# Kernel optimization log

Measured on AMD Instinct MI355X. Metric: run time of the kernel, lower is better.

## Reference

```python
import jax, jax.numpy as jnp
import numpy as np

B, N, DIM, H, D, S = 4, 16384, 256, 8, 64, 64
INNER = H * D


def setup_inputs() -> dict:
    key = jax.random.key(0)
    ks = jax.random.split(key, 10)
    f = lambda k, shp, s: jax.random.normal(k, shp, jnp.float32) * s
    return {
        "x": jax.random.normal(ks[0], (B, N, DIM), jnp.float32),
        "Wx": f(ks[1], (INNER, DIM), 0.02), "bx": jnp.zeros((INNER,), jnp.float32),
        "Wfx": f(ks[2], (INNER, DIM), 0.02), "bfx": jnp.zeros((INNER,), jnp.float32),
        "Wslice": f(ks[3], (S, D), 0.125), "bslice": jnp.zeros((S,), jnp.float32),
        "temperature": jnp.full((1, H, 1, 1), 0.5, jnp.float32),
        "Wq": f(ks[4], (D, D), 0.125),
        "Wk": f(ks[5], (D, D), 0.125),
        "Wv": f(ks[6], (D, D), 0.125),
        "attn_scale": jnp.full((1, H, 1, 1), 10.0, jnp.float32),
        "slice_res_scale": jnp.full((1,), 0.1, jnp.float32),
        "Wout": f(ks[7], (DIM, INNER), 0.02), "bout": jnp.zeros((DIM,), jnp.float32),
    }


def reference(x, Wx, bx, Wfx, bfx, Wslice, bslice, temperature,
              Wq, Wk, Wv, attn_scale, slice_res_scale, Wout, bout):
    b, n, _ = x.shape
    # project and split heads -> [b, h, n, d]
    fx = (x @ Wfx.T + bfx).reshape(b, n, H, D).transpose(0, 2, 1, 3)
    xm = (x @ Wx.T + bx).reshape(b, n, H, D).transpose(0, 2, 1, 3)
    temp = jnp.clip(temperature, 1e-4)
    slice_logits = (xm @ Wslice.T + bslice) / temp              # [b,h,n,S]
    w = jax.nn.softmax(slice_logits, axis=-1)                   # slice weights
    slice_norm = w.sum(axis=2)                                  # [b,h,S]
    tok = jnp.einsum('bhnc,bhng->bhgc', fx, w)                  # [b,h,S,d]
    tok = tok / (slice_norm + 1e-5)[:, :, :, None]
    # small cross-slice attention (cosine, shared kv across heads)
    q = tok @ Wq.T                                              # [b,h,S,d]
    kv = tok.mean(axis=1, keepdims=True)                        # [b,1,S,d]
    k = kv @ Wk.T
    v = kv @ Wv.T
    qn = q / jnp.maximum(jnp.linalg.norm(q, axis=-1, keepdims=True), 1e-12)
    kn = k / jnp.maximum(jnp.linalg.norm(k, axis=-1, keepdims=True), 1e-12)
    logits = jnp.einsum('bhgd,bzsd->bhgs', qn, kn) * attn_scale  # z==1 broadcast
    attn = jax.nn.softmax(logits, axis=-1)
    out_tok = jnp.einsum('bhgs,bzsd->bhgd', attn, v)
    out_tok = out_tok + slice_res_scale * tok
    # broadcast slice tokens back to points
    out_x = jnp.einsum('bhgc,bhng->bhnc', out_tok, w)           # [b,h,n,d]
    out_x = out_x.transpose(0, 2, 1, 3).reshape(b, n, H * D)
    return out_x @ Wout.T + bout
```

## Files before the change

kernel.cpp:

```cpp
#include <hip/hip_runtime.h>
#include <math.h>

#define BQ   4
#define NTOK 16384
#define DIMM 256
#define HH   8
#define DDIM 64
#define SSL  64
#define INNERD 512
#define BN_TOK (BQ*NTOK)

typedef __attribute__((ext_vector_type(8))) short short8;
typedef __attribute__((ext_vector_type(4))) float f32x4;

__device__ inline float bf2f(unsigned short u) {
    union { float f; unsigned int i; } v; v.i = ((unsigned int)u) << 16; return v.f;
}
__device__ inline unsigned short f2bf(float f) {
    union { float f; unsigned int i; } v; v.f = f;
    unsigned int r = v.i + 0x7FFFu + ((v.i >> 16) & 1u);
    return (unsigned short)(r >> 16);
}

__device__ __forceinline__ void gl_lds16(const void* g, void* l) {
    __builtin_amdgcn_global_load_lds(
        (const __attribute__((address_space(1))) unsigned int*)g,
        (__attribute__((address_space(3))) unsigned int*)l, 16, 0, 0);
}

#define WAIT_VM(N) asm volatile("s_waitcnt vmcnt(" #N ")" ::: "memory")
#define WAIT_LGKM0() asm volatile("s_waitcnt lgkmcnt(0)" ::: "memory")

__global__ void k_prep(const float* __restrict__ Wx, const float* __restrict__ bx,
                       const float* __restrict__ Wfx, const float* __restrict__ bfx,
                       const float* __restrict__ Wslice, const float* __restrict__ bslice,
                       unsigned short* __restrict__ Wcatb, float* __restrict__ bcat)
{
    int row = blockIdx.x;
    int t = threadIdx.x;
    if (row < 512) {
        for (int c = t; c < 256; c += 64) Wcatb[row*256 + c] = f2bf(Wfx[row*256 + c]);
        if (t == 0) bcat[row] = bfx[row];
    } else {
        int r = row - 512, h = r >> 6, s = r & 63;
        for (int c = t; c < 256; c += 64) {
            float acc = 0.f;
            for (int d = 0; d < 64; ++d)
                acc += Wslice[s*64 + d] * Wx[(h*64 + d)*256 + c];
            Wcatb[row*256 + c] = f2bf(acc);
        }
        if (t == 0) {
            float acc = bslice[s];
            for (int d = 0; d < 64; ++d) acc += Wslice[s*64 + d] * bx[h*64 + d];
            bcat[row] = acc;
        }
    }
}

__global__ void k_xcast(const float* __restrict__ x, unsigned short* __restrict__ xb)
{
    size_t i = ((size_t)blockIdx.x*256 + threadIdx.x)*8;
    float4 a = *(const float4*)(x + i);
    float4 b = *(const float4*)(x + i + 4);
    *(ushort4*)(xb + i)     = make_ushort4(f2bf(a.x), f2bf(a.y), f2bf(a.z), f2bf(a.w));
    *(ushort4*)(xb + i + 4) = make_ushort4(f2bf(b.x), f2bf(b.y), f2bf(b.z), f2bf(b.w));
}

__global__ __launch_bounds__(256) void k_gemm1(
    const unsigned short* __restrict__ Xb, const unsigned short* __restrict__ Wb,
    const float* __restrict__ bias, const float* __restrict__ temperature,
    unsigned short* __restrict__ fx_t, unsigned short* __restrict__ wbuf)
{
    __shared__ unsigned short As[2][128*32];
    __shared__ unsigned short Bs[2][128*32];
    int bid = blockIdx.x;
    int xcd = bid & 7;
    int inner = bid >> 3;
    int rt = xcd*64 + (inner >> 3);
    int ct = inner & 7;
    int m0 = rt*128, n0 = ct*128;
    int tid = threadIdx.x;
    int lane = tid & 63, w = tid >> 6;
    int wr = w >> 1, wc = w & 1;
    int lr = lane & 15, lq = lane >> 4;

    f32x4 acc[4][4];
#pragma unroll
    for (int i = 0; i < 4; i++)
#pragma unroll
        for (int j = 0; j < 4; j++) acc[i][j] = (f32x4)(0.f);

    int r0 = tid >> 2, kq0 = (tid & 3) * 8;

    auto stage = [&](int buf, int k0) {
        gl_lds16(Xb + (size_t)(m0 + r0)*256 + k0 + kq0,      &As[buf][(size_t)tid*8]);
        gl_lds16(Xb + (size_t)(m0 + 64 + r0)*256 + k0 + kq0, &As[buf][(size_t)(tid+256)*8]);
        gl_lds16(Wb + (size_t)(n0 + r0)*256 + k0 + kq0,      &Bs[buf][(size_t)tid*8]);
        gl_lds16(Wb + (size_t)(n0 + 64 + r0)*256 + k0 + kq0, &Bs[buf][(size_t)(tid+256)*8]);
    };

    stage(0, 0);
    stage(1, 32);
    int cur = 0;
#pragma unroll
    for (int t = 0; t < 8; ++t) {
        if (t < 7) { WAIT_VM(4); } else { WAIT_VM(0); }
        __builtin_amdgcn_s_barrier();
        short8 af[4], bf[4];
#pragma unroll
        for (int i = 0; i < 4; i++) {
            af[i] = *(const short8*)&As[cur][(wr*64 + i*16 + lr)*32 + lq*8];
            bf[i] = *(const short8*)&Bs[cur][(wc*64 + i*16 + lr)*32 + lq*8];
        }
        WAIT_LGKM0();
        __builtin_amdgcn_sched_barrier(0);
        __builtin_amdgcn_s_barrier();
        if (t < 6) stage(cur, (t + 2) * 32);
#pragma unroll
        for (int i = 0; i < 4; i++)
#pragma unroll
            for (int j = 0; j < 4; j++)
                acc[i][j] = __builtin_amdgcn_mfma_f32_16x16x32_bf16(af[i], bf[j], acc[i][j], 0, 0, 0);
        cur ^= 1;
    }

    float bv[4];
#pragma unroll
    for (int j = 0; j < 4; j++) bv[j] = bias[n0 + wc*64 + j*16 + lr];

    if (n0 < 512) {
        int h = (n0 + wc*64) >> 6;
        int batch = m0 >> 14;
#pragma unroll
        for (int i = 0; i < 4; i++) {
            int tokbase = m0 + wr*64 + i*16 + lq*4;
            int nloc = tokbase & (NTOK-1);
#pragma unroll
            for (int j = 0; j < 4; j++) {
                int d = j*16 + lr;
                ushort4 pk = make_ushort4(
                    f2bf(acc[i][j][0] + bv[j]), f2bf(acc[i][j][1] + bv[j]),
                    f2bf(acc[i][j][2] + bv[j]), f2bf(acc[i][j][3] + bv[j]));
                *(ushort4*)(fx_t + ((size_t)(batch*8 + h)*64 + d)*NTOK + nloc) = pk;
            }
        }
    } else {
        int h = (n0 - 512 + wc*64) >> 6;
        float it = 1.f / fmaxf(temperature[h], 1e-4f);
        int colbase = (n0 - 512) + wc*64;
#pragma unroll
        for (int i = 0; i < 4; i++) {
            int tokbase = m0 + wr*64 + i*16 + lq*4;
#pragma unroll
            for (int r = 0; r < 4; r++) {
                float v[4];
#pragma unroll
                for (int j = 0; j < 4; j++) v[j] = (acc[i][j][r] + bv[j]) * it;
                float mx = fmaxf(fmaxf(v[0], v[1]), fmaxf(v[2], v[3]));
                mx = fmaxf(mx, __shfl_xor(mx, 1));
                mx = fmaxf(mx, __shfl_xor(mx, 2));
                mx = fmaxf(mx, __shfl_xor(mx, 4));
                mx = fmaxf(mx, __shfl_xor(mx, 8));
                float e[4], sm = 0.f;
#pragma unroll
                for (int j = 0; j < 4; j++) { e[j] = __expf(v[j] - mx); sm += e[j]; }
                sm += __shfl_xor(sm, 1);
                sm += __shfl_xor(sm, 2);
                sm += __shfl_xor(sm, 4);
                sm += __shfl_xor(sm, 8);
                float inv = 1.f / sm;
                size_t rowoff = (size_t)(tokbase + r)*512 + colbase + lr;
#pragma unroll
                for (int j = 0; j < 4; j++)
                    wbuf[rowoff + j*16] = f2bf(e[j] * inv);
            }
        }
    }
}

__global__ __launch_bounds__(256) void k_tok(
    const unsigned short* __restrict__ wbuf, const unsigned short* __restrict__ fx_t,
    float* __restrict__ tok_acc, float* __restrict__ norm_acc)
{
    __shared__ unsigned short As[2][32*64];
    __shared__ unsigned short Bs[2][64*32];
    int chunk = blockIdx.x;
    int bh = blockIdx.y;
    int b = bh >> 3, h = bh & 7;
    int n0 = chunk * 512;
    int tid = threadIdx.x;
    int lane = tid & 63, w = tid >> 6;
    int lr = lane & 15, lq = lane >> 4;

    f32x4 acc[4];
#pragma unroll
    for (int j = 0; j < 4; j++) acc[j] = (f32x4)(0.f);
    float nacc = 0.f;

    const unsigned short* wsrc =
        wbuf + ((size_t)(b*NTOK + n0 + (tid >> 3)))*512 + h*64 + (tid & 7)*8;
    const unsigned short* fsrc =
        fx_t + ((size_t)bh*64 + (tid >> 2))*NTOK + n0 + (tid & 3)*8;

    auto stage = [&](int buf, int kk) {
        gl_lds16(wsrc + (size_t)kk*512, &As[buf][(size_t)tid*8]);
        gl_lds16(fsrc + kk,             &Bs[buf][(size_t)tid*8]);
    };

    stage(0, 0);
    stage(1, 32);
    int cur = 0;
#pragma unroll
    for (int t = 0; t < 16; ++t) {
        if (t < 15) { WAIT_VM(2); } else { WAIT_VM(0); }
        __builtin_amdgcn_s_barrier();
        const unsigned short* arow = &As[cur][w*16 + lr];
        short8 af;
#pragma unroll
        for (int e = 0; e < 8; ++e)
            af[e] = (short)arow[(lq*8 + e)*64];
        short8 bfv[4];
#pragma unroll
        for (int j = 0; j < 4; j++)
            bfv[j] = *(const short8*)&Bs[cur][(j*16 + lr)*32 + lq*8];
        WAIT_LGKM0();
        __builtin_amdgcn_sched_barrier(0);
        __builtin_amdgcn_s_barrier();
        if (t < 14) stage(cur, (t + 2) * 32);

        float ns = 0.f;
#pragma unroll
        for (int e = 0; e < 8; ++e) ns += bf2f((unsigned short)af[e]);
        nacc += ns;
#pragma unroll
        for (int j = 0; j < 4; j++)
            acc[j] = __builtin_amdgcn_mfma_f32_16x16x32_bf16(af, bfv[j], acc[j], 0, 0, 0);
        cur ^= 1;
    }

#pragma unroll
    for (int j = 0; j < 4; j++) {
        int d = j*16 + lr;
#pragma unroll
        for (int r = 0; r < 4; r++) {
            int s = w*16 + lq*4 + r;
            atomicAdd(&tok_acc[((size_t)bh*64 + s)*64 + d], acc[j][r]);
        }
    }
    nacc += __shfl_xor(nacc, 16);
    nacc += __shfl_xor(nacc, 32);
    if (lq == 0)
        atomicAdd(&norm_acc[bh*64 + w*16 + lr], nacc);
}

__global__ __launch_bounds__(256) void k_kv(
    const float* __restrict__ tok, const float* __restrict__ norm,
    const float* __restrict__ Wk, const float* __restrict__ Wv,
    float* __restrict__ kn_out, float* __restrict__ v_out)
{
    __shared__ float KV[64][65];
    __shared__ float TMP[64][65];
    __shared__ float rn[64];
    __shared__ float inv[8][64];
    int b = blockIdx.x, tid = threadIdx.x;
    for (int idx = tid; idx < 512; idx += 256) {
        int h = idx >> 6, s = idx & 63;
        inv[h][s] = 1.f / (norm[(b*8 + h)*64 + s] + 1e-5f);
    }
    __syncthreads();
    for (int idx = tid; idx < 4096; idx += 256) {
        int s = idx >> 6;
        float acc = 0.f;
        for (int h = 0; h < 8; ++h)
            acc += tok[((size_t)(b*8 + h))*4096 + idx] * inv[h][s];
        KV[s][idx & 63] = acc * 0.125f;
    }
    __syncthreads();
    for (int idx = tid; idx < 4096; idx += 256) {
        int s = idx >> 6, d = idx & 63;
        float a = 0.f;
        for (int e = 0; e < 64; ++e) a += KV[s][e] * Wk[d*64 + e];
        TMP[s][d] = a;
    }
    __syncthreads();
    if (tid < 64) {
        float a = 0.f;
        for (int d = 0; d < 64; ++d) { float x = TMP[tid][d]; a += x*x; }
        rn[tid] = fmaxf(sqrtf(a), 1e-12f);
    }
    __syncthreads();
    for (int idx = tid; idx < 4096; idx += 256) {
        int s = idx >> 6, d = idx & 63;
        kn_out[(size_t)b*4096 + idx] = TMP[s][d] / rn[s];
    }
    for (int idx = tid; idx < 4096; idx += 256) {
        int s = idx >> 6, d = idx & 63;
        float a = 0.f;
        for (int e = 0; e < 64; ++e) a += KV[s][e] * Wv[d*64 + e];
        v_out[(size_t)b*4096 + idx] = a;
    }
}

__global__ __launch_bounds__(256) void k_attn(
    const float* __restrict__ tok, const float* __restrict__ norm,
    const float* __restrict__ Wq,
    const float* __restrict__ kn, const float* __restrict__ vbuf,
    const float* __restrict__ attn_scale, const float* __restrict__ srs,
    float* __restrict__ out_tok)
{
    __shared__ float TN[64][65];
    __shared__ float Q[64][65];
    __shared__ float KN[64][65];
    __shared__ float L[64][65];
    __shared__ float rn[64];
    int h = blockIdx.x & 7, b = blockIdx.x >> 3;
    int bh = b*8 + h;
    int tid = threadIdx.x;
    for (int idx = tid; idx < 4096; idx += 256) {
        int g = idx >> 6;
        TN[g][idx & 63] = tok[(size_t)bh*4096 + idx] / (norm[bh*64 + g] + 1e-5f);
        KN[g][idx & 63] = kn[(size_t)b*4096 + idx];
    }
    __syncthreads();
    for (int idx = tid; idx < 4096; idx += 256) {
        int g = idx >> 6, d = idx & 63;
        float a = 0.f;
        for (int e = 0; e < 64; ++e) a += TN[g][e] * Wq[d*64 + e];
        Q[g][d] = a;
    }
    __syncthreads();
    if (tid < 64) {
        float a = 0.f;
        for (int d = 0; d < 64; ++d) { float x = Q[tid][d]; a += x*x; }
        rn[tid] = fmaxf(sqrtf(a), 1e-12f);
    }
    __syncthreads();
    float scale = attn_scale[h];
    for (int idx = tid; idx < 4096; idx += 256) {
        int g = idx >> 6, s = idx & 63;
        float a = 0.f;
        for (int e = 0; e < 64; ++e) a += Q[g][e] * KN[s][e];
        L[g][s] = a / rn[g] * scale;
    }
    __syncthreads();
    if (tid < 64) {
        float mx = -1e30f;
        for (int s = 0; s < 64; ++s) mx = fmaxf(mx, L[tid][s]);
        float sm = 0.f;
        for (int s = 0; s < 64; ++s) { float e = expf(L[tid][s]-mx); L[tid][s] = e; sm += e; }
        float ivv = 1.f/sm;
        for (int s = 0; s < 64; ++s) L[tid][s] *= ivv;
    }
    __syncthreads();
    float srsv = srs[0];
    for (int idx = tid; idx < 4096; idx += 256) {
        int g = idx >> 6, d = idx & 63;
        float a = 0.f;
        for (int s = 0; s < 64; ++s) a += L[g][s] * vbuf[(size_t)b*4096 + s*64 + d];
        out_tok[(size_t)bh*4096 + idx] = a + srsv * TN[g][d];
    }
}

__global__ __launch_bounds__(256) void k_mt(
    const float* __restrict__ out_tok, const float* __restrict__ Wout,
    unsigned short* __restrict__ MTb)
{
    __shared__ float Wt[64][68];
    __shared__ float Ot[64][68];
    int jt = blockIdx.x, h = blockIdx.y, b = blockIdx.z;
    int j0 = jt * 64;
    int tid = threadIdx.x;
    int tx = tid & 15, ty = tid >> 4;
#pragma unroll
    for (int i = 0; i < 4; i++) {
        int flat = tid + i*256;
        int r = flat >> 4;
        int c4 = (flat & 15) * 4;
        float4 wv = *(const float4*)(Wout + (size_t)(j0+r)*512 + h*64 + c4);
        Wt[c4+0][r]=wv.x; Wt[c4+1][r]=wv.y; Wt[c4+2][r]=wv.z; Wt[c4+3][r]=wv.w;
        float4 ov = *(const float4*)(out_tok + ((size_t)(b*8+h)*64 + r)*64 + c4);
        Ot[c4+0][r]=ov.x; Ot[c4+1][r]=ov.y; Ot[c4+2][r]=ov.z; Ot[c4+3][r]=ov.w;
    }
    __syncthreads();
    float acc[4][4] = {{0.f}};
#pragma unroll 8
    for (int d = 0; d < 64; ++d) {
        float av[4], bv[4];
        *(float4*)av = *(const float4*)&Wt[d][ty*4];
        *(float4*)bv = *(const float4*)&Ot[d][tx*4];
#pragma unroll
        for (int i = 0; i < 4; i++)
#pragma unroll
            for (int j = 0; j < 4; j++) acc[i][j] += av[i]*bv[j];
    }
#pragma unroll
    for (int i = 0; i < 4; i++) {
        int j = j0 + ty*4 + i;
#pragma unroll
        for (int jj = 0; jj < 4; jj++) {
            int s = tx*4 + jj;
            MTb[((size_t)(b*256) + j)*512 + h*64 + s] = f2bf(acc[i][jj]);
        }
    }
}

__global__ __launch_bounds__(256) void k_gemm2(
    const unsigned short* __restrict__ A, const unsigned short* __restrict__ Ball,
    const float* __restrict__ bias, float* __restrict__ C)
{
    __shared__ unsigned short As[2][128*32];
    __shared__ unsigned short Bs[2][128*32];
    int bid = blockIdx.x;
    int xcd = bid & 7;
    int inner = bid >> 3;
    int rt = xcd*64 + (inner >> 1);
    int ct = inner & 1;
    int m0 = rt*128, n0 = ct*128;
    const unsigned short* Bm = Ball + (size_t)(m0 >> 14) * 256 * 512;
    int tid = threadIdx.x;
    int lane = tid & 63, w = tid >> 6;
    int wr = w >> 1, wc = w & 1;
    int lr = lane & 15, lq = lane >> 4;

    f32x4 acc[4][4];
#pragma unroll
    for (int i = 0; i < 4; i++)
#pragma unroll
        for (int j = 0; j < 4; j++) acc[i][j] = (f32x4)(0.f);

    int r0 = tid >> 2, kq0 = (tid & 3) * 8;

    auto stage = [&](int buf, int k0) {
        gl_lds16(A + (size_t)(m0 + r0)*512 + k0 + kq0,       &As[buf][(size_t)tid*8]);
        gl_lds16(A + (size_t)(m0 + 64 + r0)*512 + k0 + kq0,  &As[buf][(size_t)(tid+256)*8]);
        gl_lds16(Bm + (size_t)(n0 + r0)*512 + k0 + kq0,      &Bs[buf][(size_t)tid*8]);
        gl_lds16(Bm + (size_t)(n0 + 64 + r0)*512 + k0 + kq0, &Bs[buf][(size_t)(tid+256)*8]);
    };

    stage(0, 0);
    stage(1, 32);
    int cur = 0;
#pragma unroll
    for (int t = 0; t < 16; ++t) {
        if (t < 15) { WAIT_VM(4); } else { WAIT_VM(0); }
        __builtin_amdgcn_s_barrier();
        short8 af[4], bf[4];
#pragma unroll
        for (int i = 0; i < 4; i++) {
            af[i] = *(const short8*)&As[cur][(wr*64 + i*16 + lr)*32 + lq*8];
            bf[i] = *(const short8*)&Bs[cur][(wc*64 + i*16 + lr)*32 + lq*8];
        }
        WAIT_LGKM0();
        __builtin_amdgcn_sched_barrier(0);
        __builtin_amdgcn_s_barrier();
        if (t < 14) stage(cur, (t + 2) * 32);
#pragma unroll
        for (int i = 0; i < 4; i++)
#pragma unroll
            for (int j = 0; j < 4; j++)
                acc[i][j] = __builtin_amdgcn_mfma_f32_16x16x32_bf16(af[i], bf[j], acc[i][j], 0, 0, 0);
        cur ^= 1;
    }

#pragma unroll
    for (int j = 0; j < 4; j++) {
        int n = n0 + wc*64 + j*16 + lr;
        float bv = bias[n];
#pragma unroll
        for (int i = 0; i < 4; i++) {
            int mrow = m0 + wr*64 + i*16 + lq*4;
#pragma unroll
            for (int r = 0; r < 4; r++)
                C[(size_t)(mrow + r)*256 + n] = acc[i][j][r] + bv;
        }
    }
}

extern "C" void kernel_launch(void* const* d_in, const int* in_sizes, int n_in,
                              void* d_out, int out_size, void* d_ws, size_t ws_size,
                              hipStream_t stream)
{
    const float* x      = (const float*)d_in[0];
    const float* Wx     = (const float*)d_in[1];
    const float* bx     = (const float*)d_in[2];
    const float* Wfx    = (const float*)d_in[3];
    const float* bfx    = (const float*)d_in[4];
    const float* Wslice = (const float*)d_in[5];
    const float* bslice = (const float*)d_in[6];
    const float* temperature = (const float*)d_in[7];
    const float* Wq     = (const float*)d_in[8];
    const float* Wk     = (const float*)d_in[9];
    const float* Wv     = (const float*)d_in[10];
    const float* attn_scale = (const float*)d_in[11];
    const float* srs    = (const float*)d_in[12];
    const float* Wout   = (const float*)d_in[13];
    const float* bout   = (const float*)d_in[14];
    float* out = (float*)d_out;
    float* ws  = (float*)d_ws;

    float* tok  = ws + 0;
    float* norm = ws + 131072;
    float* bcat = ws + 133120;
    float* kn   = ws + 134144;
    float* vb   = ws + 150528;
    float* ot   = ws + 166912;
    unsigned short* Wcatb = (unsigned short*)(ws + 297984);
    unsigned short* MTb   = (unsigned short*)(ws + 429056);
    unsigned short* xb    = (unsigned short*)(ws + 691200);
    unsigned short* wbuf  = (unsigned short*)(ws + 9079808);
    unsigned short* fx_t  = (unsigned short*)d_out;

    hipMemsetAsync(tok, 0, 133120 * sizeof(float), stream);
    k_prep<<<1024, 64, 0, stream>>>(Wx, bx, Wfx, bfx, Wslice, bslice, Wcatb, bcat);
    k_xcast<<<8192, 256, 0, stream>>>(x, xb);
    k_gemm1<<<4096, 256, 0, stream>>>(xb, Wcatb, bcat, temperature, fx_t, wbuf);
    k_tok<<<dim3(32, 32), 256, 0, stream>>>(wbuf, fx_t, tok, norm);
    k_kv<<<4, 256, 0, stream>>>(tok, norm, Wk, Wv, kn, vb);
    k_attn<<<32, 256, 0, stream>>>(tok, norm, Wq, kn, vb, attn_scale, srs, ot);
    k_mt<<<dim3(4, 8, 4), 256, 0, stream>>>(ot, Wout, MTb);
    k_gemm2<<<1024, 256, 0, stream>>>(wbuf, MTb, bout, out);
}
```

Measured before the change: 368.7 us.

## Fuse fx projection into slice-token kernel and swizzle LDS layouts

```diff
diff --git a/kernel.cpp b/kernel.cpp
--- a/kernel.cpp
+++ b/kernel.cpp
@@ -69,20 +69,21 @@
 __global__ __launch_bounds__(256) void k_gemm1(
     const unsigned short* __restrict__ Xb, const unsigned short* __restrict__ Wb,
     const float* __restrict__ bias, const float* __restrict__ temperature,
-    unsigned short* __restrict__ fx_t, unsigned short* __restrict__ wbuf)
+    unsigned short* __restrict__ wbuf)
 {
     __shared__ unsigned short As[2][128*32];
     __shared__ unsigned short Bs[2][128*32];
     int bid = blockIdx.x;
     int xcd = bid & 7;
     int inner = bid >> 3;
-    int rt = xcd*64 + (inner >> 3);
-    int ct = inner & 7;
+    int rt = xcd*64 + (inner >> 2);
+    int ct = inner & 3;
     int m0 = rt*128, n0 = ct*128;
     int tid = threadIdx.x;
     int lane = tid & 63, w = tid >> 6;
     int wr = w >> 1, wc = w & 1;
     int lr = lane & 15, lq = lane >> 4;
+    int lqs = lq ^ ((lr >> 1) & 3);
 
     f32x4 acc[4][4];
 #pragma unroll
@@ -90,13 +91,14 @@
 #pragma unroll
         for (int j = 0; j < 4; j++) acc[i][j] = (f32x4)(0.f);
 
-    int r0 = tid >> 2, kq0 = (tid & 3) * 8;
+    int r0 = tid >> 2;
+    int kswz = (((tid & 3) ^ ((tid >> 3) & 3))) * 8;
 
     auto stage = [&](int buf, int k0) {
-        gl_lds16(Xb + (size_t)(m0 + r0)*256 + k0 + kq0,      &As[buf][(size_t)tid*8]);
-        gl_lds16(Xb + (size_t)(m0 + 64 + r0)*256 + k0 + kq0, &As[buf][(size_t)(tid+256)*8]);
-        gl_lds16(Wb + (size_t)(n0 + r0)*256 + k0 + kq0,      &Bs[buf][(size_t)tid*8]);
-        gl_lds16(Wb + (size_t)(n0 + 64 + r0)*256 + k0 + kq0, &Bs[buf][(size_t)(tid+256)*8]);
+        gl_lds16(Xb + (size_t)(m0 + r0)*256 + k0 + kswz,          &As[buf][(size_t)tid*8]);
+        gl_lds16(Xb + (size_t)(m0 + 64 + r0)*256 + k0 + kswz,     &As[buf][(size_t)(tid+256)*8]);
+        gl_lds16(Wb + (size_t)(512 + n0 + r0)*256 + k0 + kswz,    &Bs[buf][(size_t)tid*8]);
+        gl_lds16(Wb + (size_t)(512 + n0 + 64 + r0)*256 + k0 + kswz, &Bs[buf][(size_t)(tid+256)*8]);
     };
 
     stage(0, 0);
@@ -109,8 +111,8 @@
         short8 af[4], bf[4];
 #pragma unroll
         for (int i = 0; i < 4; i++) {
-            af[i] = *(const short8*)&As[cur][(wr*64 + i*16 + lr)*32 + lq*8];
-            bf[i] = *(const short8*)&Bs[cur][(wc*64 + i*16 + lr)*32 + lq*8];
+            af[i] = *(const short8*)&As[cur][(wr*64 + i*16 + lr)*32 + lqs*8];
+            bf[i] = *(const short8*)&Bs[cur][(wc*64 + i*16 + lr)*32 + lqs*8];
         }
         WAIT_LGKM0();
         __builtin_amdgcn_sched_barrier(0);
@@ -126,116 +128,136 @@
 
     float bv[4];
 #pragma unroll
-    for (int j = 0; j < 4; j++) bv[j] = bias[n0 + wc*64 + j*16 + lr];
-
-    if (n0 < 512) {
-        int h = (n0 + wc*64) >> 6;
-        int batch = m0 >> 14;
-#pragma unroll
-        for (int i = 0; i < 4; i++) {
-            int tokbase = m0 + wr*64 + i*16 + lq*4;
-            int nloc = tokbase & (NTOK-1);
-#pragma unroll
-            for (int j = 0; j < 4; j++) {
-                int d = j*16 + lr;
-                ushort4 pk = make_ushort4(
-                    f2bf(acc[i][j][0] + bv[j]), f2bf(acc[i][j][1] + bv[j]),
-                    f2bf(acc[i][j][2] + bv[j]), f2bf(acc[i][j][3] + bv[j]));
-                *(ushort4*)(fx_t + ((size_t)(batch*8 + h)*64 + d)*NTOK + nloc) = pk;
-            }
-        }
-    } else {
-        int h = (n0 - 512 + wc*64) >> 6;
-        float it = 1.f / fmaxf(temperature[h], 1e-4f);
-        int colbase = (n0 - 512) + wc*64;
-#pragma unroll
-        for (int i = 0; i < 4; i++) {
-            int tokbase = m0 + wr*64 + i*16 + lq*4;
-#pragma unroll
-            for (int r = 0; r < 4; r++) {
-                float v[4];
-#pragma unroll
-                for (int j = 0; j < 4; j++) v[j] = (acc[i][j][r] + bv[j]) * it;
-                float mx = fmaxf(fmaxf(v[0], v[1]), fmaxf(v[2], v[3]));
-                mx = fmaxf(mx, __shfl_xor(mx, 1));
-                mx = fmaxf(mx, __shfl_xor(mx, 2));
-                mx = fmaxf(mx, __shfl_xor(mx, 4));
-                mx = fmaxf(mx, __shfl_xor(mx, 8));
-                float e[4], sm = 0.f;
-#pragma unroll
-                for (int j = 0; j < 4; j++) { e[j] = __expf(v[j] - mx); sm += e[j]; }
-                sm += __shfl_xor(sm, 1);
-                sm += __shfl_xor(sm, 2);
-                sm += __shfl_xor(sm, 4);
-                sm += __shfl_xor(sm, 8);
-                float inv = 1.f / sm;
-                size_t rowoff = (size_t)(tokbase + r)*512 + colbase + lr;
-#pragma unroll
-                for (int j = 0; j < 4; j++)
-                    wbuf[rowoff + j*16] = f2bf(e[j] * inv);
-            }
+    for (int j = 0; j < 4; j++) bv[j] = bias[512 + n0 + wc*64 + j*16 + lr];
+
+    int h = (n0 + wc*64) >> 6;
+    float it = 1.f / fmaxf(temperature[h], 1e-4f);
+    int colbase = n0 + wc*64;
+#pragma unroll
+    for (int i = 0; i < 4; i++) {
+        int tokbase = m0 + wr*64 + i*16 + lq*4;
+#pragma unroll
+        for (int r = 0; r < 4; r++) {
+            float v[4];
+#pragma unroll
+            for (int j = 0; j < 4; j++) v[j] = (acc[i][j][r] + bv[j]) * it;
+            float mx = fmaxf(fmaxf(v[0], v[1]), fmaxf(v[2], v[3]));
+            mx = fmaxf(mx, __shfl_xor(mx, 1));
+            mx = fmaxf(mx, __shfl_xor(mx, 2));
+            mx = fmaxf(mx, __shfl_xor(mx, 4));
+            mx = fmaxf(mx, __shfl_xor(mx, 8));
+            float e[4], sm = 0.f;
+#pragma unroll
+            for (int j = 0; j < 4; j++) { e[j] = __expf(v[j] - mx); sm += e[j]; }
+            sm += __shfl_xor(sm, 1);
+            sm += __shfl_xor(sm, 2);
+            sm += __shfl_xor(sm, 4);
+            sm += __shfl_xor(sm, 8);
+            float inv = 1.f / sm;
+            size_t rowoff = (size_t)(tokbase + r)*512 + colbase + lr;
+#pragma unroll
+            for (int j = 0; j < 4; j++)
+                wbuf[rowoff + j*16] = f2bf(e[j] * inv);
         }
     }
 }
 
 __global__ __launch_bounds__(256) void k_tok(
-    const unsigned short* __restrict__ wbuf, const unsigned short* __restrict__ fx_t,
+    const unsigned short* __restrict__ Xb, const unsigned short* __restrict__ Wcatb,
+    const float* __restrict__ bcat, const unsigned short* __restrict__ wbuf,
     float* __restrict__ tok_acc, float* __restrict__ norm_acc)
 {
-    __shared__ unsigned short As[2][32*64];
-    __shared__ unsigned short Bs[2][64*32];
+    __shared__ unsigned short As[128*32];
+    __shared__ unsigned short Bs[64*32];
+    __shared__ unsigned short FX[64*128];
+    __shared__ unsigned short WL[128*64];
     int chunk = blockIdx.x;
     int bh = blockIdx.y;
     int b = bh >> 3, h = bh & 7;
-    int n0 = chunk * 512;
+    size_t grow = (size_t)b*NTOK + chunk*128;
     int tid = threadIdx.x;
     int lane = tid & 63, w = tid >> 6;
     int lr = lane & 15, lq = lane >> 4;
-
-    f32x4 acc[4];
-#pragma unroll
-    for (int j = 0; j < 4; j++) acc[j] = (f32x4)(0.f);
+    int lqs = lq ^ ((lr >> 1) & 3);
+
+#pragma unroll
+    for (int p = 0; p < 4; ++p) {
+        int e = p*256 + tid;
+        gl_lds16(wbuf + (grow + (e >> 3))*512 + h*64 + (e & 7)*8,
+                 &WL[(size_t)e*8]);
+    }
+
+    f32x4 facc[2][4];
+#pragma unroll
+    for (int i = 0; i < 2; i++)
+#pragma unroll
+        for (int j = 0; j < 4; j++) facc[i][j] = (f32x4)(0.f);
+
+    int r0 = tid >> 2;
+    int kswz = (((tid & 3) ^ ((tid >> 3) & 3))) * 8;
+
+    for (int k0 = 0; k0 < 256; k0 += 32) {
+        __syncthreads();
+        gl_lds16(Xb + (grow + r0)*256 + k0 + kswz,            &As[(size_t)tid*8]);
+        gl_lds16(Xb + (grow + 64 + r0)*256 + k0 + kswz,       &As[(size_t)(tid+256)*8]);
+        gl_lds16(Wcatb + (size_t)(h*64 + r0)*256 + k0 + kswz, &Bs[(size_t)tid*8]);
+        __syncthreads();
+        short8 af[2], bf[4];
+#pragma unroll
+        for (int i = 0; i < 2; i++)
+            af[i] = *(const short8*)&As[(w*32 + i*16 + lr)*32 + lqs*8];
+#pragma unroll
+        for (int j = 0; j < 4; j++)
+            bf[j] = *(const short8*)&Bs[(j*16 + lr)*32 + lqs*8];
+#pragma unroll
+        for (int i = 0; i < 2; i++)
+#pragma unroll
+            for (int j = 0; j < 4; j++)
+                facc[i][j] = __builtin_amdgcn_mfma_f32_16x16x32_bf16(af[i], bf[j], facc[i][j], 0, 0, 0);
+    }
+
+    float fbv[4];
+#pragma unroll
+    for (int j = 0; j < 4; j++) fbv[j] = bcat[h*64 + j*16 + lr];
+#pragma unroll
+    for (int i = 0; i < 2; i++)
+#pragma unroll
+        for (int j = 0; j < 4; j++) {
+            int d = j*16 + lr;
+#pragma unroll
+            for (int r = 0; r < 4; r++) {
+                int tok = w*32 + i*16 + lq*4 + r;
+                int ss = (tok >> 3) ^ ((d >> 1) & 3);
+                FX[d*128 + ss*8 + (tok & 7)] = f2bf(facc[i][j][r] + fbv[j]);
+            }
+        }
+    __syncthreads();
+
+    f32x4 racc[4];
+#pragma unroll
+    for (int j = 0; j < 4; j++) racc[j] = (f32x4)(0.f);
     float nacc = 0.f;
 
-    const unsigned short* wsrc =
-        wbuf + ((size_t)(b*NTOK + n0 + (tid >> 3)))*512 + h*64 + (tid & 7)*8;
-    const unsigned short* fsrc =
-        fx_t + ((size_t)bh*64 + (tid >> 2))*NTOK + n0 + (tid & 3)*8;
-
-    auto stage = [&](int buf, int kk) {
-        gl_lds16(wsrc + (size_t)kk*512, &As[buf][(size_t)tid*8]);
-        gl_lds16(fsrc + kk,             &Bs[buf][(size_t)tid*8]);
-    };
-
-    stage(0, 0);
-    stage(1, 32);
-    int cur = 0;
-#pragma unroll
-    for (int t = 0; t < 16; ++t) {
-        if (t < 15) { WAIT_VM(2); } else { WAIT_VM(0); }
-        __builtin_amdgcn_s_barrier();
-        const unsigned short* arow = &As[cur][w*16 + lr];
+#pragma unroll
+    for (int kk = 0; kk < 4; ++kk) {
         short8 af;
-#pragma unroll
-        for (int e = 0; e < 8; ++e)
-            af[e] = (short)arow[(lq*8 + e)*64];
+        float ns = 0.f;
+#pragma unroll
+        for (int e = 0; e < 8; ++e) {
+            unsigned short u = WL[(kk*32 + lq*8 + e)*64 + w*16 + lr];
+            af[e] = (short)u;
+            ns += bf2f(u);
+        }
+        nacc += ns;
         short8 bfv[4];
 #pragma unroll
+        for (int j = 0; j < 4; j++) {
+            int ss = (kk*4 + lq) ^ ((lr >> 1) & 3);
+            bfv[j] = *(const short8*)&FX[(j*16 + lr)*128 + ss*8];
+        }
+#pragma unroll
         for (int j = 0; j < 4; j++)
-            bfv[j] = *(const short8*)&Bs[cur][(j*16 + lr)*32 + lq*8];
-        WAIT_LGKM0();
-        __builtin_amdgcn_sched_barrier(0);
-        __builtin_amdgcn_s_barrier();
-        if (t < 14) stage(cur, (t + 2) * 32);
-
-        float ns = 0.f;
-#pragma unroll
-        for (int e = 0; e < 8; ++e) ns += bf2f((unsigned short)af[e]);
-        nacc += ns;
-#pragma unroll
-        for (int j = 0; j < 4; j++)
-            acc[j] = __builtin_amdgcn_mfma_f32_16x16x32_bf16(af, bfv[j], acc[j], 0, 0, 0);
-        cur ^= 1;
+            racc[j] = __builtin_amdgcn_mfma_f32_16x16x32_bf16(af, bfv[j], racc[j], 0, 0, 0);
     }
 
 #pragma unroll
@@ -244,7 +266,7 @@
 #pragma unroll
         for (int r = 0; r < 4; r++) {
             int s = w*16 + lq*4 + r;
-            atomicAdd(&tok_acc[((size_t)bh*64 + s)*64 + d], acc[j][r]);
+            atomicAdd(&tok_acc[((size_t)bh*64 + s)*64 + d], racc[j][r]);
         }
     }
     nacc += __shfl_xor(nacc, 16);
@@ -421,6 +443,7 @@
     int lane = tid & 63, w = tid >> 6;
     int wr = w >> 1, wc = w & 1;
     int lr = lane & 15, lq = lane >> 4;
+    int lqs = lq ^ ((lr >> 1) & 3);
 
     f32x4 acc[4][4];
 #pragma unroll
@@ -428,13 +451,14 @@
 #pragma unroll
         for (int j = 0; j < 4; j++) acc[i][j] = (f32x4)(0.f);
 
-    int r0 = tid >> 2, kq0 = (tid & 3) * 8;
+    int r0 = tid >> 2;
+    int kswz = (((tid & 3) ^ ((tid >> 3) & 3))) * 8;
 
     auto stage = [&](int buf, int k0) {
-        gl_lds16(A + (size_t)(m0 + r0)*512 + k0 + kq0,       &As[buf][(size_t)tid*8]);
-        gl_lds16(A + (size_t)(m0 + 64 + r0)*512 + k0 + kq0,  &As[buf][(size_t)(tid+256)*8]);
-        gl_lds16(Bm + (size_t)(n0 + r0)*512 + k0 + kq0,      &Bs[buf][(size_t)tid*8]);
-        gl_lds16(Bm + (size_t)(n0 + 64 + r0)*512 + k0 + kq0, &Bs[buf][(size_t)(tid+256)*8]);
+        gl_lds16(A + (size_t)(m0 + r0)*512 + k0 + kswz,       &As[buf][(size_t)tid*8]);
+        gl_lds16(A + (size_t)(m0 + 64 + r0)*512 + k0 + kswz,  &As[buf][(size_t)(tid+256)*8]);
+        gl_lds16(Bm + (size_t)(n0 + r0)*512 + k0 + kswz,      &Bs[buf][(size_t)tid*8]);
+        gl_lds16(Bm + (size_t)(n0 + 64 + r0)*512 + k0 + kswz, &Bs[buf][(size_t)(tid+256)*8]);
     };
 
     stage(0, 0);
@@ -447,8 +471,8 @@
         short8 af[4], bf[4];
 #pragma unroll
         for (int i = 0; i < 4; i++) {
-            af[i] = *(const short8*)&As[cur][(wr*64 + i*16 + lr)*32 + lq*8];
-            bf[i] = *(const short8*)&Bs[cur][(wc*64 + i*16 + lr)*32 + lq*8];
+            af[i] = *(const short8*)&As[cur][(wr*64 + i*16 + lr)*32 + lqs*8];
+            bf[i] = *(const short8*)&Bs[cur][(wc*64 + i*16 + lr)*32 + lqs*8];
         }
         WAIT_LGKM0();
         __builtin_amdgcn_sched_barrier(0);
@@ -508,13 +532,12 @@
     unsigned short* MTb   = (unsigned short*)(ws + 429056);
     unsigned short* xb    = (unsigned short*)(ws + 691200);
     unsigned short* wbuf  = (unsigned short*)(ws + 9079808);
-    unsigned short* fx_t  = (unsigned short*)d_out;
 
     hipMemsetAsync(tok, 0, 133120 * sizeof(float), stream);
     k_prep<<<1024, 64, 0, stream>>>(Wx, bx, Wfx, bfx, Wslice, bslice, Wcatb, bcat);
     k_xcast<<<8192, 256, 0, stream>>>(x, xb);
-    k_gemm1<<<4096, 256, 0, stream>>>(xb, Wcatb, bcat, temperature, fx_t, wbuf);
-    k_tok<<<dim3(32, 32), 256, 0, stream>>>(wbuf, fx_t, tok, norm);
+    k_gemm1<<<2048, 256, 0, stream>>>(xb, Wcatb, bcat, temperature, wbuf);
+    k_tok<<<dim3(128, 32), 256, 0, stream>>>(xb, Wcatb, bcat, wbuf, tok, norm);
     k_kv<<<4, 256, 0, stream>>>(tok, norm, Wk, Wv, kn, vb);
     k_attn<<<32, 256, 0, stream>>>(tok, norm, Wq, kn, vb, attn_scale, srs, ot);
     k_mt<<<dim3(4, 8, 4), 256, 0, stream>>>(ot, Wout, MTb);
```

New measurement: 397.6 us. 1.08x slower.

## Use 512-thread GEMM blocks with smaller per-wave tiles and XOR-swizzled LDS

Applied to the files above, without the earlier changes.

```diff
diff --git a/kernel.cpp b/kernel.cpp
--- a/kernel.cpp
+++ b/kernel.cpp
@@ -66,7 +66,7 @@
     *(ushort4*)(xb + i + 4) = make_ushort4(f2bf(b.x), f2bf(b.y), f2bf(b.z), f2bf(b.w));
 }
 
-__global__ __launch_bounds__(256) void k_gemm1(
+__global__ __launch_bounds__(512, 4) void k_gemm1(
     const unsigned short* __restrict__ Xb, const unsigned short* __restrict__ Wb,
     const float* __restrict__ bias, const float* __restrict__ temperature,
     unsigned short* __restrict__ fx_t, unsigned short* __restrict__ wbuf)
@@ -81,22 +81,22 @@
     int m0 = rt*128, n0 = ct*128;
     int tid = threadIdx.x;
     int lane = tid & 63, w = tid >> 6;
-    int wr = w >> 1, wc = w & 1;
+    int wrow = w >> 1, wcol = w & 1;
     int lr = lane & 15, lq = lane >> 4;
-
-    f32x4 acc[4][4];
-#pragma unroll
-    for (int i = 0; i < 4; i++)
+    int lqs = lq ^ ((lr >> 1) & 3);
+
+    f32x4 acc[2][4];
+#pragma unroll
+    for (int i = 0; i < 2; i++)
 #pragma unroll
         for (int j = 0; j < 4; j++) acc[i][j] = (f32x4)(0.f);
 
-    int r0 = tid >> 2, kq0 = (tid & 3) * 8;
+    int r0 = tid >> 2;
+    int kswz = (((tid & 3) ^ ((tid >> 3) & 3))) * 8;
 
     auto stage = [&](int buf, int k0) {
-        gl_lds16(Xb + (size_t)(m0 + r0)*256 + k0 + kq0,      &As[buf][(size_t)tid*8]);
-        gl_lds16(Xb + (size_t)(m0 + 64 + r0)*256 + k0 + kq0, &As[buf][(size_t)(tid+256)*8]);
-        gl_lds16(Wb + (size_t)(n0 + r0)*256 + k0 + kq0,      &Bs[buf][(size_t)tid*8]);
-        gl_lds16(Wb + (size_t)(n0 + 64 + r0)*256 + k0 + kq0, &Bs[buf][(size_t)(tid+256)*8]);
+        gl_lds16(Xb + (size_t)(m0 + r0)*256 + k0 + kswz, &As[buf][(size_t)tid*8]);
+        gl_lds16(Wb + (size_t)(n0 + r0)*256 + k0 + kswz, &Bs[buf][(size_t)tid*8]);
     };
 
     stage(0, 0);
@@ -104,20 +104,21 @@
     int cur = 0;
 #pragma unroll
     for (int t = 0; t < 8; ++t) {
-        if (t < 7) { WAIT_VM(4); } else { WAIT_VM(0); }
+        if (t < 7) { WAIT_VM(2); } else { WAIT_VM(0); }
         __builtin_amdgcn_s_barrier();
-        short8 af[4], bf[4];
-#pragma unroll
-        for (int i = 0; i < 4; i++) {
-            af[i] = *(const short8*)&As[cur][(wr*64 + i*16 + lr)*32 + lq*8];
-            bf[i] = *(const short8*)&Bs[cur][(wc*64 + i*16 + lr)*32 + lq*8];
-        }
+        short8 af[2], bf[4];
+#pragma unroll
+        for (int i = 0; i < 2; i++)
+            af[i] = *(const short8*)&As[cur][(wrow*32 + i*16 + lr)*32 + lqs*8];
+#pragma unroll
+        for (int j = 0; j < 4; j++)
+            bf[j] = *(const short8*)&Bs[cur][(wcol*64 + j*16 + lr)*32 + lqs*8];
         WAIT_LGKM0();
         __builtin_amdgcn_sched_barrier(0);
         __builtin_amdgcn_s_barrier();
         if (t < 6) stage(cur, (t + 2) * 32);
 #pragma unroll
-        for (int i = 0; i < 4; i++)
+        for (int i = 0; i < 2; i++)
 #pragma unroll
             for (int j = 0; j < 4; j++)
                 acc[i][j] = __builtin_amdgcn_mfma_f32_16x16x32_bf16(af[i], bf[j], acc[i][j], 0, 0, 0);
@@ -126,14 +127,14 @@
 
     float bv[4];
 #pragma unroll
-    for (int j = 0; j < 4; j++) bv[j] = bias[n0 + wc*64 + j*16 + lr];
+    for (int j = 0; j < 4; j++) bv[j] = bias[n0 + wcol*64 + j*16 + lr];
 
     if (n0 < 512) {
-        int h = (n0 + wc*64) >> 6;
+        int h = (n0 + wcol*64) >> 6;
         int batch = m0 >> 14;
 #pragma unroll
-        for (int i = 0; i < 4; i++) {
-            int tokbase = m0 + wr*64 + i*16 + lq*4;
+        for (int i = 0; i < 2; i++) {
+            int tokbase = m0 + wrow*32 + i*16 + lq*4;
             int nloc = tokbase & (NTOK-1);
 #pragma unroll
             for (int j = 0; j < 4; j++) {
@@ -145,12 +146,12 @@
             }
         }
     } else {
-        int h = (n0 - 512 + wc*64) >> 6;
+        int h = (n0 - 512 + wcol*64) >> 6;
         float it = 1.f / fmaxf(temperature[h], 1e-4f);
-        int colbase = (n0 - 512) + wc*64;
-#pragma unroll
-        for (int i = 0; i < 4; i++) {
-            int tokbase = m0 + wr*64 + i*16 + lq*4;
+        int colbase = (n0 - 512) + wcol*64;
+#pragma unroll
+        for (int i = 0; i < 2; i++) {
+            int tokbase = m0 + wrow*32 + i*16 + lq*4;
 #pragma unroll
             for (int r = 0; r < 4; r++) {
                 float v[4];
@@ -191,6 +192,7 @@
     int tid = threadIdx.x;
     int lane = tid & 63, w = tid >> 6;
     int lr = lane & 15, lq = lane >> 4;
+    int lqs = lq ^ ((lr >> 1) & 3);
 
     f32x4 acc[4];
 #pragma unroll
@@ -199,8 +201,9 @@
 
     const unsigned short* wsrc =
         wbuf + ((size_t)(b*NTOK + n0 + (tid >> 3)))*512 + h*64 + (tid & 7)*8;
+    int kswz = (((tid & 3) ^ ((tid >> 3) & 3))) * 8;
     const unsigned short* fsrc =
-        fx_t + ((size_t)bh*64 + (tid >> 2))*NTOK + n0 + (tid & 3)*8;
+        fx_t + ((size_t)bh*64 + (tid >> 2))*NTOK + n0 + kswz;
 
     auto stage = [&](int buf, int kk) {
         gl_lds16(wsrc + (size_t)kk*512, &As[buf][(size_t)tid*8]);
@@ -222,7 +225,7 @@
         short8 bfv[4];
 #pragma unroll
         for (int j = 0; j < 4; j++)
-            bfv[j] = *(const short8*)&Bs[cur][(j*16 + lr)*32 + lq*8];
+            bfv[j] = *(const short8*)&Bs[cur][(j*16 + lr)*32 + lqs*8];
         WAIT_LGKM0();
         __builtin_amdgcn_sched_barrier(0);
         __builtin_amdgcn_s_barrier();
@@ -404,7 +407,7 @@
     }
 }
 
-__global__ __launch_bounds__(256) void k_gemm2(
+__global__ __launch_bounds__(512, 4) void k_gemm2(
     const unsigned short* __restrict__ A, const unsigned short* __restrict__ Ball,
     const float* __restrict__ bias, float* __restrict__ C)
 {
@@ -419,22 +422,22 @@
     const unsigned short* Bm = Ball + (size_t)(m0 >> 14) * 256 * 512;
     int tid = threadIdx.x;
     int lane = tid & 63, w = tid >> 6;
-    int wr = w >> 1, wc = w & 1;
+    int wrow = w >> 1, wcol = w & 1;
     int lr = lane & 15, lq = lane >> 4;
-
-    f32x4 acc[4][4];
-#pragma unroll
-    for (int i = 0; i < 4; i++)
+    int lqs = lq ^ ((lr >> 1) & 3);
+
+    f32x4 acc[2][4];
+#pragma unroll
+    for (int i = 0; i < 2; i++)
 #pragma unroll
         for (int j = 0; j < 4; j++) acc[i][j] = (f32x4)(0.f);
 
-    int r0 = tid >> 2, kq0 = (tid & 3) * 8;
+    int r0 = tid >> 2;
+    int kswz = (((tid & 3) ^ ((tid >> 3) & 3))) * 8;
 
     auto stage = [&](int buf, int k0) {
-        gl_lds16(A + (size_t)(m0 + r0)*512 + k0 + kq0,       &As[buf][(size_t)tid*8]);
-        gl_lds16(A + (size_t)(m0 + 64 + r0)*512 + k0 + kq0,  &As[buf][(size_t)(tid+256)*8]);
-        gl_lds16(Bm + (size_t)(n0 + r0)*512 + k0 + kq0,      &Bs[buf][(size_t)tid*8]);
-        gl_lds16(Bm + (size_t)(n0 + 64 + r0)*512 + k0 + kq0, &Bs[buf][(size_t)(tid+256)*8]);
+        gl_lds16(A + (size_t)(m0 + r0)*512 + k0 + kswz,  &As[buf][(size_t)tid*8]);
+        gl_lds16(Bm + (size_t)(n0 + r0)*512 + k0 + kswz, &Bs[buf][(size_t)tid*8]);
     };
 
     stage(0, 0);
@@ -442,20 +445,21 @@
     int cur = 0;
 #pragma unroll
     for (int t = 0; t < 16; ++t) {
-        if (t < 15) { WAIT_VM(4); } else { WAIT_VM(0); }
+        if (t < 15) { WAIT_VM(2); } else { WAIT_VM(0); }
         __builtin_amdgcn_s_barrier();
-        short8 af[4], bf[4];
-#pragma unroll
-        for (int i = 0; i < 4; i++) {
-            af[i] = *(const short8*)&As[cur][(wr*64 + i*16 + lr)*32 + lq*8];
-            bf[i] = *(const short8*)&Bs[cur][(wc*64 + i*16 + lr)*32 + lq*8];
-        }
+        short8 af[2], bf[4];
+#pragma unroll
+        for (int i = 0; i < 2; i++)
+            af[i] = *(const short8*)&As[cur][(wrow*32 + i*16 + lr)*32 + lqs*8];
+#pragma unroll
+        for (int j = 0; j < 4; j++)
+            bf[j] = *(const short8*)&Bs[cur][(wcol*64 + j*16 + lr)*32 + lqs*8];
         WAIT_LGKM0();
         __builtin_amdgcn_sched_barrier(0);
         __builtin_amdgcn_s_barrier();
         if (t < 14) stage(cur, (t + 2) * 32);
 #pragma unroll
-        for (int i = 0; i < 4; i++)
+        for (int i = 0; i < 2; i++)
 #pragma unroll
             for (int j = 0; j < 4; j++)
                 acc[i][j] = __builtin_amdgcn_mfma_f32_16x16x32_bf16(af[i], bf[j], acc[i][j], 0, 0, 0);
@@ -464,11 +468,11 @@
 
 #pragma unroll
     for (int j = 0; j < 4; j++) {
-        int n = n0 + wc*64 + j*16 + lr;
+        int n = n0 + wcol*64 + j*16 + lr;
         float bv = bias[n];
 #pragma unroll
-        for (int i = 0; i < 4; i++) {
-            int mrow = m0 + wr*64 + i*16 + lq*4;
+        for (int i = 0; i < 2; i++) {
+            int mrow = m0 + wrow*32 + i*16 + lq*4;
 #pragma unroll
             for (int r = 0; r < 4; r++)
                 C[(size_t)(mrow + r)*256 + n] = acc[i][j][r] + bv;
@@ -513,10 +517,10 @@
     hipMemsetAsync(tok, 0, 133120 * sizeof(float), stream);
     k_prep<<<1024, 64, 0, stream>>>(Wx, bx, Wfx, bfx, Wslice, bslice, Wcatb, bcat);
     k_xcast<<<8192, 256, 0, stream>>>(x, xb);
-    k_gemm1<<<4096, 256, 0, stream>>>(xb, Wcatb, bcat, temperature, fx_t, wbuf);
+    k_gemm1<<<4096, 512, 0, stream>>>(xb, Wcatb, bcat, temperature, fx_t, wbuf);
     k_tok<<<dim3(32, 32), 256, 0, stream>>>(wbuf, fx_t, tok, norm);
     k_kv<<<4, 256, 0, stream>>>(tok, norm, Wk, Wv, kn, vb);
     k_attn<<<32, 256, 0, stream>>>(tok, norm, Wq, kn, vb, attn_scale, srs, ot);
     k_mt<<<dim3(4, 8, 4), 256, 0, stream>>>(ot, Wout, MTb);
-    k_gemm2<<<1024, 256, 0, stream>>>(wbuf, MTb, bout, out);
-}
+    k_gemm2<<<1024, 512, 0, stream>>>(wbuf, MTb, bout, out);
+}
```

New measurement: 365.5 us. Within noise of the previous version (-0.9%).
